# Kernel tuning notes

Measured on AMD Instinct MI355X. Metric: run time of the kernel, lower is better.

The kernel has to match this reference:

```python
import jax, jax.numpy as jnp
import numpy as np

NUM_NODES = 100000


def setup_inputs() -> dict:
    key = jax.random.key(0)
    k1, k2, k3, k4, k5 = jax.random.split(key, 5)
    E = 3200000
    features = jax.random.normal(k1, (NUM_NODES, 32), dtype=jnp.float32)
    edge_srcs = jax.random.randint(k2, (E,), 0, NUM_NODES, dtype=jnp.int32)
    edge_dsts = jax.random.randint(k3, (E,), 0, NUM_NODES, dtype=jnp.int32)
    edge_weights = jax.random.uniform(k4, (E,), dtype=jnp.float32)
    kernels = jax.random.normal(k5, (32, 32), dtype=jnp.float32) * 0.1
    biases = jnp.zeros((32,), dtype=jnp.float32)
    return {
        "features": features,
        "edge_srcs": edge_srcs,
        "edge_dsts": edge_dsts,
        "edge_weights": edge_weights,
        "kernels": kernels,
        "biases": biases,
    }


def reference(features, edge_srcs, edge_dsts, edge_weights, kernels, biases):
    num_nodes = features.shape[0]
    # dense transform: [N, F_in] @ [F_in, F_out] -> [N, F_out]
    h = features @ kernels
    # per-src degrees via segment sum of ones, clipped to >= 1
    deg = jax.ops.segment_sum(
        jnp.ones_like(edge_srcs, dtype=h.dtype), edge_srcs, num_segments=num_nodes
    )
    norm = jnp.clip(deg, 1.0, None) ** -0.5  # [N]
    # symmetric-normalized edge weights: norm[src] * w * norm[dst]
    w = norm[edge_srcs] * edge_weights * norm[edge_dsts]  # [E]
    # gather dst features, scale, scatter-add into src rows
    nbr = h[edge_dsts] * w[:, None]  # [E, F_out]
    reduced = jax.ops.segment_sum(nbr, edge_srcs, num_segments=num_nodes)
    return reduced + biases
```

## Files before the change

### kernel.cpp

```cpp
#include <hip/hip_runtime.h>
#include <hip/hip_fp16.h>

#define FDIM 32
#define BSH 7
#define BNODES 128
#define NBMAX 1024
#define CHUNK 8192
#define NCMAX 512
#define RCAP 4608
#define SCAP 5120

typedef unsigned int u32;
typedef unsigned short u16;

#define BFLO(u) __uint_as_float((u) << 16)
#define BFHI(u) __uint_as_float((u) & 0xFFFF0000u)

union HCV { __half h; u16 u; };
__device__ __forceinline__ u16 f32_f16b(float f) { HCV c; c.h = __float2half(f); return c.u; }
__device__ __forceinline__ float f16b_f32(u32 b) { HCV c; c.u = (u16)b; return __half2float(c.h); }

__device__ __forceinline__ void acc8(float4& p0, float4& p1, float w, uint4 h) {
    p0.x = fmaf(w, BFLO(h.x), p0.x);
    p0.y = fmaf(w, BFHI(h.x), p0.y);
    p0.z = fmaf(w, BFLO(h.y), p0.z);
    p0.w = fmaf(w, BFHI(h.y), p0.w);
    p1.x = fmaf(w, BFLO(h.z), p1.x);
    p1.y = fmaf(w, BFHI(h.z), p1.y);
    p1.z = fmaf(w, BFLO(h.w), p1.z);
    p1.w = fmaf(w, BFHI(h.w), p1.w);
}

__global__ __launch_bounds__(1024, 8) void k1b(const int* __restrict__ srcs,
                                               const int* __restrict__ dsts,
                                               const float* __restrict__ ew,
                                               u32* __restrict__ offsT,
                                               u32* __restrict__ rkey,
                                               u16* __restrict__ rwh,
                                               int E, int NB, int nch) {
    __shared__ __align__(16) u32 skey[CHUNK];
    __shared__ __align__(16) u16 swv[CHUNK];
    __shared__ u32 lh[NBMAX];
    __shared__ u32 wsum[16];
    int t = threadIdx.x, c = blockIdx.x;
    int base = c * CHUNK;
    int end = base + CHUNK; if (end > E) end = E;
    int nloc = end - base;
    int i0 = t * 8;
    bool full = (i0 + 8 <= nloc);
    int sv[8], dv[8];
    float wv[8];
    u32 rk[8];
    if (full) {
        int4 a  = ((const int4*)(srcs + base))[t * 2];
        int4 b2 = ((const int4*)(srcs + base))[t * 2 + 1];
        int4 d0 = ((const int4*)(dsts + base))[t * 2];
        int4 d1 = ((const int4*)(dsts + base))[t * 2 + 1];
        float4 w0 = ((const float4*)(ew + base))[t * 2];
        float4 w1 = ((const float4*)(ew + base))[t * 2 + 1];
        sv[0]=a.x; sv[1]=a.y; sv[2]=a.z; sv[3]=a.w; sv[4]=b2.x; sv[5]=b2.y; sv[6]=b2.z; sv[7]=b2.w;
        dv[0]=d0.x; dv[1]=d0.y; dv[2]=d0.z; dv[3]=d0.w; dv[4]=d1.x; dv[5]=d1.y; dv[6]=d1.z; dv[7]=d1.w;
        wv[0]=w0.x; wv[1]=w0.y; wv[2]=w0.z; wv[3]=w0.w; wv[4]=w1.x; wv[5]=w1.y; wv[6]=w1.z; wv[7]=w1.w;
    } else {
#pragma unroll
        for (int k = 0; k < 8; ++k) {
            int i = i0 + k;
            bool v = i < nloc;
            sv[k] = v ? srcs[base + i] : 0;
            dv[k] = v ? dsts[base + i] : 0;
            wv[k] = v ? ew[base + i] : 0.f;
        }
    }
    for (int i = t; i < NB; i += 1024) lh[i] = 0u;
    __syncthreads();
    if (full) {
#pragma unroll
        for (int k = 0; k < 8; ++k) rk[k] = atomicAdd(&lh[sv[k] >> BSH], 1u);
    } else {
#pragma unroll
        for (int k = 0; k < 8; ++k) {
            bool v = (i0 + k) < nloc;
            rk[k] = v ? atomicAdd(&lh[sv[k] >> BSH], 1u) : 0u;
        }
    }
    __syncthreads();
    int lane = t & 63, w = t >> 6;
    u32 v = (t < NB) ? lh[t] : 0u;
    u32 inc = v;
#pragma unroll
    for (int d = 1; d < 64; d <<= 1) {
        u32 o = __shfl_up(inc, (unsigned)d, 64);
        if (lane >= d) inc += o;
    }
    if (lane == 63) wsum[w] = inc;
    __syncthreads();
    u32 woff = 0;
    for (int i = 0; i < w; ++i) woff += wsum[i];
    inc += woff;
    u32 ex = inc - v;
    if (t < NB) { offsT[(size_t)t * nch + c] = ex; lh[t] = ex; }
    if (t == 0) offsT[(size_t)NB * nch + c] = (u32)nloc;
    __syncthreads();
    if (full) {
#pragma unroll
        for (int k = 0; k < 8; ++k) {
            int s = sv[k];
            u32 pos = lh[s >> BSH] + rk[k];
            skey[pos] = ((u32)(s & (BNODES - 1)) << 17) | (u32)dv[k];
            swv[pos] = f32_f16b(wv[k]);
        }
    } else {
#pragma unroll
        for (int k = 0; k < 8; ++k) {
            if ((i0 + k) < nloc) {
                int s = sv[k];
                u32 pos = lh[s >> BSH] + rk[k];
                skey[pos] = ((u32)(s & (BNODES - 1)) << 17) | (u32)dv[k];
                swv[pos] = f32_f16b(wv[k]);
            }
        }
    }
    __syncthreads();
    ((uint4*)(rkey + (size_t)base))[t]        = ((const uint4*)skey)[t];
    ((uint4*)(rkey + (size_t)base))[t + 1024] = ((const uint4*)skey)[t + 1024];
    ((uint4*)(rwh + (size_t)base))[t]         = ((const uint4*)swv)[t];
}

__global__ __launch_bounds__(512) void k_sort(const u32* __restrict__ rkey,
                                              const u16* __restrict__ rwh,
                                              const u32* __restrict__ offsT,
                                              u32* __restrict__ srec,
                                              u32* __restrict__ nodemeta,
                                              int N, int NB, int nch) {
    __shared__ __align__(16) u32 ssrec[SCAP];
    __shared__ u32 sbase[NCMAX];
    __shared__ u16 runid[RCAP];
    __shared__ u32 lcnt[BNODES];
    __shared__ u32 lexoff[BNODES];
    __shared__ uint2 ovf[512];
    __shared__ u32 ovn;
    __shared__ u32 wsum[8];
    __shared__ u32 ws2[2];
    __shared__ u32 stot;
    int b = blockIdx.x, t = threadIdx.x;
    int base_n = b << BSH;
    if (t < BNODES) lcnt[t] = 0u;
    if (t == 0) ovn = 0u;
    u32 rl = 0u, s0 = 0u;
    if (t < nch) {
        s0 = offsT[(size_t)b * nch + t];
        rl = offsT[(size_t)(b + 1) * nch + t] - s0;
    }
    int lane = t & 63, w = t >> 6;
    u32 inc = rl;
#pragma unroll
    for (int d = 1; d < 64; d <<= 1) {
        u32 o = __shfl_up(inc, (unsigned)d, 64);
        if (lane >= d) inc += o;
    }
    if (lane == 63) wsum[w] = inc;
    __syncthreads();
    u32 woff = 0;
    for (int i = 0; i < w; ++i) woff += wsum[i];
    inc += woff;
    if (t < nch) {
        u32 pl0 = inc - rl;
        sbase[t] = (u32)t * CHUNK + s0 - pl0;
        u32 p = pl0 < RCAP ? pl0 : RCAP;
        u32 e = pl0 + rl; if (e > RCAP) e = RCAP;
        for (; p < e; ++p) runid[p] = (u16)t;
    }
    if (t == nch - 1) stot = inc;
    __syncthreads();
    u32 tot = stot; if (tot > RCAP) tot = RCAP;
    u32 keyv[8], whv[8], rankv[8]; bool val[8];
#pragma unroll
    for (int i = 0; i < 8; ++i) {
        u32 g = (u32)t + ((u32)i << 9);
        val[i] = g < tot;
        keyv[i] = 0u; whv[i] = 0u; rankv[i] = 0u;
        if (val[i]) {
            int r = runid[g];
            u32 idx = sbase[r] + g;
            keyv[i] = rkey[(size_t)idx];
            whv[i] = rwh[(size_t)idx];
        }
    }
#pragma unroll
    for (int i = 0; i < 8; ++i)
        if (val[i]) rankv[i] = atomicAdd(&lcnt[keyv[i] >> 17], 1u);
    for (u32 g = (u32)t + 4096u; g < tot; g += 512u) {
        int r = runid[g];
        u32 idx = sbase[r] + g;
        u32 key = rkey[(size_t)idx];
        u32 wh = rwh[(size_t)idx];
        u32 rk2 = atomicAdd(&lcnt[key >> 17], 1u);
        u32 oi = atomicAdd(&ovn, 1u);
        if (oi < 512u) ovf[oi] = make_uint2(key, (u32)wh | (rk2 << 16));
    }
    __syncthreads();
    u32 d = 0u, pad = 0u, inc2 = 0u;
    if (t < BNODES) {
        d = lcnt[t];
        pad = (d + 3u) & ~3u;
        inc2 = pad;
    }
    if (t < 128) {
#pragma unroll
        for (int dd = 1; dd < 64; dd <<= 1) {
            u32 o = __shfl_up(inc2, (unsigned)dd, 64);
            if ((t & 63) >= dd) inc2 += o;
        }
        if ((t & 63) == 63) ws2[t >> 6] = inc2;
    }
    __syncthreads();
    if (t < 128) {
        if (t >= 64) inc2 += ws2[0];
        u32 ex = inc2 - pad;
        lexoff[t] = ex;
        int n = base_n + t;
        if (n < N) nodemeta[n] = ex | (d << 16);
    }
    __syncthreads();
#pragma unroll
    for (int i = 0; i < 8; ++i) {
        if (val[i]) {
            u32 slot = keyv[i] >> 17;
            u32 pos = lexoff[slot] + rankv[i];
            if (pos < SCAP) ssrec[pos] = ((keyv[i] & 0x1FFFFu) << 15) | ((u32)whv[i] & 0x7FFFu);
        }
    }
    u32 no = ovn; if (no > 512u) no = 512u;
    for (u32 i = t; i < no; i += 512u) {
        uint2 q = ovf[i];
        u32 slot = q.x >> 17;
        u32 pos = lexoff[slot] + (q.y >> 16);
        if (pos < SCAP) ssrec[pos] = ((q.x & 0x1FFFFu) << 15) | (q.y & 0x7FFFu);
    }
    __syncthreads();
    u32* dst = srec + (size_t)b * SCAP;
    for (int i = t; i < SCAP / 4; i += 512) ((uint4*)dst)[i] = ((const uint4*)ssrec)[i];
}

__global__ __launch_bounds__(512) void k_gemm(const float* __restrict__ feat,
                                              const float* __restrict__ kern,
                                              const u32* __restrict__ nodemeta,
                                              u16* __restrict__ hsb,
                                              int N) {
    __shared__ float skern[FDIM * FDIM];
    __shared__ float sfeat[BNODES * FDIM];
    __shared__ float lnorm[BNODES];
    int b = blockIdx.x, t = threadIdx.x;
    for (int i = t; i < FDIM * FDIM / 4; i += 512) ((float4*)skern)[i] = ((const float4*)kern)[i];
    int base_n = b << BSH;
    int base_nf = base_n * FDIM;
    int lim = N * FDIM - base_nf; if (lim > BNODES * FDIM) lim = BNODES * FDIM;
    for (int i = t; i < (lim >> 2); i += 512) ((float4*)sfeat)[i] = ((const float4*)(feat + base_nf))[i];
    if (t < BNODES) {
        int n = base_n + t;
        u32 m = (n < N) ? nodemeta[n] : 0u;
        lnorm[t] = rsqrtf(fmaxf((float)(m >> 16), 1.0f));
    }
    __syncthreads();
    int f = t & 31, g8 = t >> 5;
    float kc[FDIM];
#pragma unroll
    for (int k = 0; k < FDIM; ++k) kc[k] = skern[k * FDIM + f];
#pragma unroll
    for (int k8 = 0; k8 < 8; ++k8) {
        int nl = g8 * 8 + k8;
        int n = base_n + nl;
        const float4* fr = (const float4*)(sfeat + nl * FDIM);
        float4 rr[8];
#pragma unroll
        for (int q = 0; q < 8; ++q) rr[q] = fr[q];
        float acc = 0.f;
#pragma unroll
        for (int q = 0; q < 8; ++q) {
            acc = fmaf(rr[q].x, kc[4 * q + 0], acc);
            acc = fmaf(rr[q].y, kc[4 * q + 1], acc);
            acc = fmaf(rr[q].z, kc[4 * q + 2], acc);
            acc = fmaf(rr[q].w, kc[4 * q + 3], acc);
        }
        float x = lnorm[nl] * acc;
        u32 u = __float_as_uint(x);
        u = (u + 0x7FFFu + ((u >> 16) & 1u)) >> 16;
        if (n < N) hsb[(size_t)n * FDIM + f] = (u16)u;
    }
}

__global__ __launch_bounds__(512) void k2(const u32* __restrict__ srec,
                                          const u32* __restrict__ nodemeta,
                                          const u16* __restrict__ hsb,
                                          const float* __restrict__ bias,
                                          float* __restrict__ out,
                                          int N, int NB) {
    __shared__ u32 loff[BNODES];
    __shared__ u32 lcnt[BNODES];
    __shared__ u32 snode[BNODES];
    __shared__ u32 lbin[128];
    __shared__ u32 ws2[2];
    int b = blockIdx.x, t = threadIdx.x;
    int base_n = b << BSH;
    if (t < BNODES) {
        int n = base_n + t;
        u32 m = (n < N) ? nodemeta[n] : 0u;
        loff[t] = m & 0xFFFFu;
        lcnt[t] = m >> 16;
    }
    if (t < 128) lbin[t] = 0u;
    __syncthreads();
    if (t < BNODES) {
        u32 len = lcnt[t];
        atomicAdd(&lbin[len > 127u ? 127u : len], 1u);
    }
    __syncthreads();
    u32 bv_ = 0u, binc = 0u;
    if (t < 128) {
        bv_ = lbin[t];
        binc = bv_;
#pragma unroll
        for (int dd = 1; dd < 64; dd <<= 1) {
            u32 o = __shfl_up(binc, (unsigned)dd, 64);
            if ((t & 63) >= dd) binc += o;
        }
        if ((t & 63) == 63) ws2[t >> 6] = binc;
    }
    __syncthreads();
    if (t < 128) {
        if (t >= 64) binc += ws2[0];
        lbin[t] = binc - bv_;
    }
    __syncthreads();
    if (t < BNODES) {
        u32 len = lcnt[t];
        u32 pos = atomicAdd(&lbin[len > 127u ? 127u : len], 1u);
        snode[pos] = (u32)t;
    }
    __syncthreads();
    int l = t & 3, g = t >> 2;
    u32 nl = snode[g];
    int n = base_n + (int)nl;
    u32 off = loff[nl];
    u32 len = lcnt[nl];
    float ns = rsqrtf(fmaxf((float)len, 1.0f));
    const u32* sp = srec + (size_t)b * SCAP + off;
    const uint4* hp4 = (const uint4*)hsb;
    float4 bv0 = ((const float4*)bias)[2 * l];
    float4 bv1 = ((const float4*)bias)[2 * l + 1];
    float4 x0 = make_float4(0.f, 0.f, 0.f, 0.f), x1 = make_float4(0.f, 0.f, 0.f, 0.f);
    float4 y0 = make_float4(0.f, 0.f, 0.f, 0.f), y1 = make_float4(0.f, 0.f, 0.f, 0.f);
    u32 j = 0;
    for (; j + 8 <= len; j += 8) {
        uint4 a = *(const uint4*)(sp + j);
        uint4 c = *(const uint4*)(sp + j + 4);
        uint4 h0 = hp4[(size_t)(a.x >> 15) * 4 + l];
        uint4 h1 = hp4[(size_t)(a.y >> 15) * 4 + l];
        uint4 h2 = hp4[(size_t)(a.z >> 15) * 4 + l];
        uint4 h3 = hp4[(size_t)(a.w >> 15) * 4 + l];
        uint4 h4 = hp4[(size_t)(c.x >> 15) * 4 + l];
        uint4 h5 = hp4[(size_t)(c.y >> 15) * 4 + l];
        uint4 h6 = hp4[(size_t)(c.z >> 15) * 4 + l];
        uint4 h7 = hp4[(size_t)(c.w >> 15) * 4 + l];
        acc8(x0, x1, f16b_f32(a.x & 0x7FFFu), h0);
        acc8(y0, y1, f16b_f32(a.y & 0x7FFFu), h1);
        acc8(x0, x1, f16b_f32(a.z & 0x7FFFu), h2);
        acc8(y0, y1, f16b_f32(a.w & 0x7FFFu), h3);
        acc8(x0, x1, f16b_f32(c.x & 0x7FFFu), h4);
        acc8(y0, y1, f16b_f32(c.y & 0x7FFFu), h5);
        acc8(x0, x1, f16b_f32(c.z & 0x7FFFu), h6);
        acc8(y0, y1, f16b_f32(c.w & 0x7FFFu), h7);
    }
    for (; j + 4 <= len; j += 4) {
        uint4 a = *(const uint4*)(sp + j);
        uint4 h0 = hp4[(size_t)(a.x >> 15) * 4 + l];
        uint4 h1 = hp4[(size_t)(a.y >> 15) * 4 + l];
        uint4 h2 = hp4[(size_t)(a.z >> 15) * 4 + l];
        uint4 h3 = hp4[(size_t)(a.w >> 15) * 4 + l];
        acc8(x0, x1, f16b_f32(a.x & 0x7FFFu), h0);
        acc8(y0, y1, f16b_f32(a.y & 0x7FFFu), h1);
        acc8(x0, x1, f16b_f32(a.z & 0x7FFFu), h2);
        acc8(y0, y1, f16b_f32(a.w & 0x7FFFu), h3);
    }
    for (; j < len; ++j) {
        u32 q = sp[j];
        uint4 h = hp4[(size_t)(q >> 15) * 4 + l];
        acc8(x0, x1, f16b_f32(q & 0x7FFFu), h);
    }
    if (n < N) {
        float4 r0, r1;
        r0.x = fmaf(ns, x0.x + y0.x, bv0.x);
        r0.y = fmaf(ns, x0.y + y0.y, bv0.y);
        r0.z = fmaf(ns, x0.z + y0.z, bv0.z);
        r0.w = fmaf(ns, x0.w + y0.w, bv0.w);
        r1.x = fmaf(ns, x1.x + y1.x, bv1.x);
        r1.y = fmaf(ns, x1.y + y1.y, bv1.y);
        r1.z = fmaf(ns, x1.z + y1.z, bv1.z);
        r1.w = fmaf(ns, x1.w + y1.w, bv1.w);
        ((float4*)(out + (size_t)n * FDIM))[2 * l] = r0;
        ((float4*)(out + (size_t)n * FDIM))[2 * l + 1] = r1;
    }
}

extern "C" void kernel_launch(void* const* d_in, const int* in_sizes, int n_in,
                              void* d_out, int out_size, void* d_ws, size_t ws_size,
                              hipStream_t stream) {
    const float* feat = (const float*)d_in[0];
    const int*   srcs = (const int*)d_in[1];
    const int*   dsts = (const int*)d_in[2];
    const float* ew   = (const float*)d_in[3];
    const float* kern = (const float*)d_in[4];
    const float* bias = (const float*)d_in[5];
    float* out = (float*)d_out;

    int N = in_sizes[0] / FDIM;
    int E = in_sizes[1];
    int NB = (N + BNODES - 1) >> BSH;
    int nchunks = (E + CHUNK - 1) / CHUNK;

    char* w = (char*)d_ws;
    u16* hsb      = (u16*)w;   w += (((size_t)N * FDIM * sizeof(u16) + 15) & ~15ull);
    u32* rkey     = (u32*)w;   w += (size_t)nchunks * CHUNK * sizeof(u32);
    u16* rwh      = (u16*)w;   w += (((size_t)nchunks * CHUNK * sizeof(u16) + 15) & ~15ull);
    u32* offsT    = (u32*)w;   w += (size_t)(NB + 1) * nchunks * sizeof(u32);
    u32* nodemeta = (u32*)w;   w += (((size_t)N * sizeof(u32) + 15) & ~15ull);
    u32* srec     = (u32*)w;   w += (size_t)NB * SCAP * sizeof(u32);

    k1b<<<nchunks, 1024, 0, stream>>>(srcs, dsts, ew, offsT, rkey, rwh, E, NB, nchunks);
    k_sort<<<NB, 512, 0, stream>>>(rkey, rwh, offsT, srec, nodemeta, N, NB, nchunks);
    k_gemm<<<NB, 512, 0, stream>>>(feat, kern, nodemeta, hsb, N);
    k2<<<NB, 512, 0, stream>>>(srec, nodemeta, hsb, bias, out, N, NB);
}
```

Before: 176.0 us.

## Fuse feature GEMM into sort kernel and split aggregation blocks in half

Merges the dense feature transform into the per-bucket sort kernel, computing the degree norm directly from local counts instead of rereading nodemeta, which removes one kernel launch. The aggregation kernel now launches twice as many 256-thread blocks, each covering 64 nodes, to improve load balance and occupancy. The fused kernel uses more shared memory, which may lower its occupancy.

```diff
diff --git a/kernel.cpp b/kernel.cpp
--- a/kernel.cpp
+++ b/kernel.cpp
@@ -126,17 +126,23 @@
     ((uint4*)(rwh + (size_t)base))[t]         = ((const uint4*)swv)[t];
 }
 
-__global__ __launch_bounds__(512) void k_sort(const u32* __restrict__ rkey,
-                                              const u16* __restrict__ rwh,
-                                              const u32* __restrict__ offsT,
-                                              u32* __restrict__ srec,
-                                              u32* __restrict__ nodemeta,
-                                              int N, int NB, int nch) {
+__global__ __launch_bounds__(512) void k_sg(const u32* __restrict__ rkey,
+                                            const u16* __restrict__ rwh,
+                                            const u32* __restrict__ offsT,
+                                            const float* __restrict__ feat,
+                                            const float* __restrict__ kern,
+                                            u32* __restrict__ srec,
+                                            u32* __restrict__ nodemeta,
+                                            u16* __restrict__ hsb,
+                                            int N, int NB, int nch) {
     __shared__ __align__(16) u32 ssrec[SCAP];
+    __shared__ float skern[FDIM * FDIM];
+    __shared__ float sfeat[BNODES * FDIM];
     __shared__ u32 sbase[NCMAX];
     __shared__ u16 runid[RCAP];
     __shared__ u32 lcnt[BNODES];
     __shared__ u32 lexoff[BNODES];
+    __shared__ float lnorm[BNODES];
     __shared__ uint2 ovf[512];
     __shared__ u32 ovn;
     __shared__ u32 wsum[8];
@@ -144,6 +150,10 @@
     __shared__ u32 stot;
     int b = blockIdx.x, t = threadIdx.x;
     int base_n = b << BSH;
+    for (int i = t; i < FDIM * FDIM / 4; i += 512) ((float4*)skern)[i] = ((const float4*)kern)[i];
+    int base_nf = base_n * FDIM;
+    int lim = N * FDIM - base_nf; if (lim > BNODES * FDIM) lim = BNODES * FDIM;
+    for (int i = t; i < (lim >> 2); i += 512) ((float4*)sfeat)[i] = ((const float4*)(feat + base_nf))[i];
     if (t < BNODES) lcnt[t] = 0u;
     if (t == 0) ovn = 0u;
     u32 rl = 0u, s0 = 0u;
@@ -218,6 +228,7 @@
         if (t >= 64) inc2 += ws2[0];
         u32 ex = inc2 - pad;
         lexoff[t] = ex;
+        lnorm[t] = rsqrtf(fmaxf((float)d, 1.0f));
         int n = base_n + t;
         if (n < N) nodemeta[n] = ex | (d << 16);
     }
@@ -240,28 +251,6 @@
     __syncthreads();
     u32* dst = srec + (size_t)b * SCAP;
     for (int i = t; i < SCAP / 4; i += 512) ((uint4*)dst)[i] = ((const uint4*)ssrec)[i];
-}
-
-__global__ __launch_bounds__(512) void k_gemm(const float* __restrict__ feat,
-                                              const float* __restrict__ kern,
-                                              const u32* __restrict__ nodemeta,
-                                              u16* __restrict__ hsb,
-                                              int N) {
-    __shared__ float skern[FDIM * FDIM];
-    __shared__ float sfeat[BNODES * FDIM];
-    __shared__ float lnorm[BNODES];
-    int b = blockIdx.x, t = threadIdx.x;
-    for (int i = t; i < FDIM * FDIM / 4; i += 512) ((float4*)skern)[i] = ((const float4*)kern)[i];
-    int base_n = b << BSH;
-    int base_nf = base_n * FDIM;
-    int lim = N * FDIM - base_nf; if (lim > BNODES * FDIM) lim = BNODES * FDIM;
-    for (int i = t; i < (lim >> 2); i += 512) ((float4*)sfeat)[i] = ((const float4*)(feat + base_nf))[i];
-    if (t < BNODES) {
-        int n = base_n + t;
-        u32 m = (n < N) ? nodemeta[n] : 0u;
-        lnorm[t] = rsqrtf(fmaxf((float)(m >> 16), 1.0f));
-    }
-    __syncthreads();
     int f = t & 31, g8 = t >> 5;
     float kc[FDIM];
 #pragma unroll
@@ -289,20 +278,21 @@
     }
 }
 
-__global__ __launch_bounds__(512) void k2(const u32* __restrict__ srec,
+__global__ __launch_bounds__(256) void k2(const u32* __restrict__ srec,
                                           const u32* __restrict__ nodemeta,
                                           const u16* __restrict__ hsb,
                                           const float* __restrict__ bias,
                                           float* __restrict__ out,
                                           int N, int NB) {
-    __shared__ u32 loff[BNODES];
-    __shared__ u32 lcnt[BNODES];
-    __shared__ u32 snode[BNODES];
+    __shared__ u32 loff[64];
+    __shared__ u32 lcnt[64];
+    __shared__ u32 snode[64];
     __shared__ u32 lbin[128];
     __shared__ u32 ws2[2];
-    int b = blockIdx.x, t = threadIdx.x;
-    int base_n = b << BSH;
-    if (t < BNODES) {
+    int b2 = blockIdx.x, t = threadIdx.x;
+    int b = b2 >> 1, half = b2 & 1;
+    int base_n = (b << BSH) + half * 64;
+    if (t < 64) {
         int n = base_n + t;
         u32 m = (n < N) ? nodemeta[n] : 0u;
         loff[t] = m & 0xFFFFu;
@@ -310,7 +300,7 @@
     }
     if (t < 128) lbin[t] = 0u;
     __syncthreads();
-    if (t < BNODES) {
+    if (t < 64) {
         u32 len = lcnt[t];
         atomicAdd(&lbin[len > 127u ? 127u : len], 1u);
     }
@@ -332,7 +322,7 @@
         lbin[t] = binc - bv_;
     }
     __syncthreads();
-    if (t < BNODES) {
+    if (t < 64) {
         u32 len = lcnt[t];
         u32 pos = atomicAdd(&lbin[len > 127u ? 127u : len], 1u);
         snode[pos] = (u32)t;
@@ -427,7 +417,6 @@
     u32* srec     = (u32*)w;   w += (size_t)NB * SCAP * sizeof(u32);
 
     k1b<<<nchunks, 1024, 0, stream>>>(srcs, dsts, ew, offsT, rkey, rwh, E, NB, nchunks);
-    k_sort<<<NB, 512, 0, stream>>>(rkey, rwh, offsT, srec, nodemeta, N, NB, nchunks);
-    k_gemm<<<NB, 512, 0, stream>>>(feat, kern, nodemeta, hsb, N);
-    k2<<<NB, 512, 0, stream>>>(srec, nodemeta, hsb, bias, out, N, NB);
+    k_sg<<<NB, 512, 0, stream>>>(rkey, rwh, offsT, feat, kern, srec, nodemeta, hsb, N, NB, nchunks);
+    k2<<<NB * 2, 256, 0, stream>>>(srec, nodemeta, hsb, bias, out, N, NB);
 }
```

Result: faster. 170.2 us (-3.3%).
